# Kernel optimization log

Measured on AMD Instinct MI355X. Metric: run time of the kernel, lower is better.

## Reference

```python
import jax, jax.numpy as jnp
import numpy as np

B, C, HK, WK = 1, 128, 32, 32
S = 4                       # upsample factor hq/hk = dilation
HQ, WQ = HK * S, WK * S
NH = 4                      # heads
HD = C // NH                # head dim
KH = KW = 7                 # odd(max(3, round(2*0.1*32)))
DH = DW = S
EPS = float(jnp.finfo(jnp.float32).eps)  # torch RMSNorm default eps for fp32


def natten_indices(L, K, D):
    """NATTEN clamped-window key indices per query position. Returns [L, K] int array."""
    NS = K // 2
    i = np.arange(L)
    if D <= 1:
        start = np.maximum(i - NS, 0) + (i + NS >= L) * (L - i - NS - 1)
    else:
        ni = i - NS * D
        imodd = i % D
        a = (L // D) * D
        b = L - a
        far = np.where(imodd < b, L - b + imodd - 2 * NS * D, a + imodd - K * D)
        start = np.where(ni < 0, imodd, np.where(i + NS * D >= L, far, ni))
    return jnp.asarray(start[:, None] + np.arange(K)[None, :] * D)


def setup_inputs() -> dict:
    key = jax.random.key(0)
    ks = jax.random.split(key, 8)
    sc = 1.0 / np.sqrt(C)
    return {
        "q": jax.random.normal(ks[0], (B, C, HQ, WQ), jnp.float32),
        "k": jax.random.normal(ks[1], (B, C, HK, WK), jnp.float32),
        "v": jax.random.normal(ks[2], (B, C, HK, WK), jnp.float32),
        "conv_w": jax.random.normal(ks[3], (C, C, 3, 3), jnp.float32) * (sc / 3.0),
        "normq_w": 1.0 + 0.02 * jax.random.normal(ks[4], (C,), jnp.float32),
        "normk_w": 1.0 + 0.02 * jax.random.normal(ks[5], (C,), jnp.float32),
        "qproj_w": jax.random.normal(ks[6], (C, C), jnp.float32) * sc,
        "qproj_b": jnp.zeros((C,), jnp.float32),
        "kproj_w": jax.random.normal(ks[7], (C, C), jnp.float32) * sc,
        "kproj_b": jnp.zeros((C,), jnp.float32),
    }


def _rmsnorm(x, w):  # x: [B,C,H,W]; RMS over channel dim
    ms = jnp.mean(x * x, axis=1, keepdims=True)
    return x * jax.lax.rsqrt(ms + EPS) * w[None, :, None, None]


def reference(q, k, v, conv_w, normq_w, normk_w, qproj_w, qproj_b, kproj_w, kproj_b):
    # 3x3 conv on q (no bias, padding=1)
    q = jax.lax.conv_general_dilated(q, conv_w, (1, 1), "SAME",
                                     dimension_numbers=("NCHW", "OIHW", "NCHW"))
    q = _rmsnorm(q, normq_w)
    k = _rmsnorm(k, normk_w)
    # 1x1 projections (Conv2d k=1 with bias)
    q = jnp.einsum("oc,bchw->bohw", qproj_w, q) + qproj_b[None, :, None, None]
    k = jnp.einsum("oc,bchw->bohw", kproj_w, k) + kproj_b[None, :, None, None]
    # nearest-exact upsample of k, v to (HQ, WQ); integer factor -> exact pixel repeat
    k = jnp.repeat(jnp.repeat(k, S, axis=2), S, axis=3)
    v = jnp.repeat(jnp.repeat(v, S, axis=2), S, axis=3)
    # NATTEN layout [B, H, W, heads, hd]
    qn = q.reshape(B, NH, HD, HQ, WQ).transpose(0, 3, 4, 1, 2)
    kn = k.reshape(B, NH, HD, HQ, WQ).transpose(0, 3, 4, 1, 2)
    vh = v.transpose(0, 2, 3, 1)  # [B,HQ,WQ,C]; V is shared (expanded) across heads.
    # channel-pad-to-8 in the original is a no-op here since C % 8 == 0.
    ih = natten_indices(HQ, KH, DH)  # [HQ, KH]
    iw = natten_indices(WQ, KW, DW)  # [WQ, KW]
    k_nb = jnp.take(jnp.take(kn, ih, axis=1), iw, axis=3)  # [B,HQ,KH,WQ,KW,NH,HD]
    v_nb = jnp.take(jnp.take(vh, ih, axis=1), iw, axis=3)  # [B,HQ,KH,WQ,KW,C]
    scale = HD ** -0.5
    logits = jnp.einsum("bijhd,bimjnhd->bijhmn", qn, k_nb) * scale
    attn = jax.nn.softmax(logits.reshape(B, HQ, WQ, NH, KH * KW), axis=-1)
    attn = attn.reshape(B, HQ, WQ, NH, KH, KW)
    # heads share V, and the block takes mean over heads at the end; the mean
    # commutes with the (linear) V-contraction, so average attention first.
    attn_mean = attn.mean(axis=3)  # [B,HQ,WQ,KH,KW]
    out = jnp.einsum("bijmn,bimjnc->bcij", attn_mean, v_nb)  # [B,C,HQ,WQ]
    return out
```

## Files before the change

kernel.cpp:

```cpp
#include <hip/hip_runtime.h>

#define EPS_ 1.1920928955078125e-07f
#define SCALE_ 0.17677669529663687f

typedef __attribute__((ext_vector_type(8))) short s8b;
typedef __attribute__((ext_vector_type(4))) float f32x4;

static __device__ __forceinline__ unsigned short f2bf(float f) {
  unsigned int u = __float_as_uint(f);
  unsigned int r = (u + 0x7fffu + ((u >> 16) & 1u)) >> 16;
  return (unsigned short)r;
}
static __device__ __forceinline__ float b2fs(short h) {
  return __uint_as_float(((unsigned int)(unsigned short)h) << 16);
}
static __device__ __forceinline__ int S_(int c) {
  return (c < 3) ? 0 : ((c > 28) ? 25 : (c - 3));
}

__global__ __launch_bounds__(256) void prep_k(
    const float* __restrict__ q_in, const float* __restrict__ k_in,
    const float* __restrict__ v_in, const float* __restrict__ conv_w,
    const float* __restrict__ normq_w, const float* __restrict__ normk_w,
    const float* __restrict__ qproj_w, const float* __restrict__ kproj_w,
    const float* __restrict__ kbias,
    unsigned short* __restrict__ qb, unsigned short* __restrict__ vb,
    unsigned short* __restrict__ kpb, unsigned short* __restrict__ wb,
    unsigned short* __restrict__ wnq) {
  __shared__ __align__(16) char smem[53504];
  unsigned short* t_l = (unsigned short*)smem;
  unsigned short* x_l = (unsigned short*)smem;
  unsigned short* wnk_l = (unsigned short*)(smem + 17408);
  float* red_l = (float*)(smem + 52224);
  float* rs_l  = (float*)(smem + 53248);
  const int b = blockIdx.x, tid = threadIdx.x;
  const int w = tid >> 6, lane = tid & 63;
  const int lm = lane & 15, kg = lane >> 4;

  if (b < 256 || (b >= 265 && b < 281)) {
    const float* src = (b < 256) ? q_in : v_in;
    const int N = (b < 256) ? 16384 : 1024;
    const int px0 = (b < 256) ? b * 64 : (b - 265) * 64;
    for (int i = tid; i < 2048; i += 256) {
      int c = i >> 4, f = i & 15;
      float4 v = *(const float4*)&src[c * N + px0 + f * 4];
      t_l[(f * 4 + 0) * 136 + c] = f2bf(v.x);
      t_l[(f * 4 + 1) * 136 + c] = f2bf(v.y);
      t_l[(f * 4 + 2) * 136 + c] = f2bf(v.z);
      t_l[(f * 4 + 3) * 136 + c] = f2bf(v.w);
    }
    __syncthreads();
    if (b < 256) {
      for (int i = tid; i < 1024; i += 256) {
        int p = i >> 4, s = i & 15;
        int px = px0 + p;
        int opx = px + 2 * (px >> 7) + 131;
        *(s8b*)&qb[opx * 128 + s * 8] = *(const s8b*)&t_l[p * 136 + s * 8];
      }
    } else {
      for (int i = tid; i < 1024; i += 256) {
        int p = i >> 4, s = i & 15;
        *(s8b*)&vb[(px0 + p) * 128 + s * 8] = *(const s8b*)&t_l[p * 136 + s * 8];
      }
    }
  } else if (b < 265) {
    int gid = (b - 256) * 256 + tid;
    s8b z = {0, 0, 0, 0, 0, 0, 0, 0};
    for (int j = gid; j < 2080; j += 2304) {
      *(s8b*)&qb[j * 8] = z;
      *(s8b*)&qb[129 * 130 * 128 + j * 8] = z;
    }
    for (int j = gid; j < 2048; j += 2304) {
      int r = (j >> 4) + 1, s = j & 15;
      *(s8b*)&qb[(r * 130) * 128 + s * 8] = z;
      *(s8b*)&qb[(r * 130 + 129) * 128 + s * 8] = z;
    }
  } else if (b < 297) {
    const int px0 = (b - 281) * 64;
    for (int i = tid; i < 2048; i += 256) {
      int c = i >> 4, f = i & 15;
      float4 v = *(const float4*)&k_in[c * 1024 + px0 + f * 4];
      x_l[(f * 4 + 0) * 136 + c] = f2bf(v.x);
      x_l[(f * 4 + 1) * 136 + c] = f2bf(v.y);
      x_l[(f * 4 + 2) * 136 + c] = f2bf(v.z);
      x_l[(f * 4 + 3) * 136 + c] = f2bf(v.w);
    }
    for (int i = tid; i < 16384; i += 256) {
      int o = i >> 7, c = i & 127;
      wnk_l[o * 136 + c] = f2bf(kproj_w[i] * normk_w[c]);
    }
    __syncthreads();
    {
      int px = tid >> 2, t4 = tid & 3;
      float ssum = 0.f;
#pragma unroll
      for (int j = 0; j < 4; j++) {
        s8b v = *(const s8b*)&x_l[px * 136 + t4 * 32 + j * 8];
#pragma unroll
        for (int e = 0; e < 8; e++) { float f = b2fs(v[e]); ssum += f * f; }
      }
      red_l[px * 4 + t4] = ssum;
    }
    __syncthreads();
    if (tid < 64)
      rs_l[tid] = rsqrtf((red_l[4 * tid] + red_l[4 * tid + 1] + red_l[4 * tid + 2] +
                          red_l[4 * tid + 3]) * (1.f / 128.f) + EPS_);
    __syncthreads();
    f32x4 acc[2][4];
#pragma unroll
    for (int a = 0; a < 2; a++)
#pragma unroll
      for (int n = 0; n < 4; n++) acc[a][n] = (f32x4){0.f, 0.f, 0.f, 0.f};
#pragma unroll
    for (int kc = 0; kc < 4; kc++) {
      s8b a0 = *(const s8b*)&wnk_l[(2 * w * 16 + lm) * 136 + kc * 32 + kg * 8];
      s8b a1 = *(const s8b*)&wnk_l[((2 * w + 1) * 16 + lm) * 136 + kc * 32 + kg * 8];
#pragma unroll
      for (int nt = 0; nt < 4; nt++) {
        s8b bf = *(const s8b*)&x_l[(nt * 16 + lm) * 136 + kc * 32 + kg * 8];
        acc[0][nt] = __builtin_amdgcn_mfma_f32_16x16x32_bf16(a0, bf, acc[0][nt], 0, 0, 0);
        acc[1][nt] = __builtin_amdgcn_mfma_f32_16x16x32_bf16(a1, bf, acc[1][nt], 0, 0, 0);
      }
    }
    __syncthreads();
#pragma unroll
    for (int mi = 0; mi < 2; mi++)
#pragma unroll
      for (int nt = 0; nt < 4; nt++)
#pragma unroll
        for (int r = 0; r < 4; r++) {
          int px = nt * 16 + lm, c = (2 * w + mi) * 16 + kg * 4 + r;
          x_l[px * 136 + c] = f2bf(kbias[c] + rs_l[px] * acc[mi][nt][r]);
        }
    __syncthreads();
    for (int i = tid; i < 1024; i += 256) {
      int px = i >> 4, s = i & 15;
      *(s8b*)&kpb[(px0 + px) * 128 + s * 8] = *(const s8b*)&x_l[px * 136 + s * 8];
    }
  } else {
    int idx = (b - 297) * 256 + tid;
    if (idx < 147456) {
      int i32 = idx & 31, r = idx >> 5;
      int oc = r & 127, r2 = r >> 7;
      int kc = r2 & 3, t = r2 >> 2;
      wb[idx] = f2bf(conv_w[oc * 1152 + (kc * 32 + i32) * 9 + t]);
    } else {
      int j = idx - 147456;
      wnq[j] = f2bf(qproj_w[j] * normq_w[j & 127]);
    }
  }
}

__global__ __launch_bounds__(256) void fused_k(
    const unsigned short* __restrict__ qb, const unsigned short* __restrict__ wb,
    const unsigned short* __restrict__ wnq, const float* __restrict__ qbias,
    const unsigned short* __restrict__ kpb, const unsigned short* __restrict__ vb,
    float* __restrict__ out) {
  __shared__ __align__(16) char smem[54528];
  unsigned short* in_l = (unsigned short*)smem;
  unsigned short* qc_l = (unsigned short*)smem;
  unsigned short* a_l  = (unsigned short*)smem;
  float* o_l = (float*)smem;
  unsigned short* v_l = (unsigned short*)(smem + 34816);
  float* red_l = (float*)(smem + 53248);
  float* rs_l  = (float*)(smem + 54272);

  const int tid = threadIdx.x;
  const int CY = blockIdx.x >> 4, CX = blockIdx.x & 15;
  const int Y0 = CY * 8, X0 = CX * 8;
  const int w = tid >> 6, lane = tid & 63;
  const int lm = lane & 15, kg = lane >> 4;

  const int sy0 = S_(2 * CY), sy1 = S_(2 * CY + 1);
  const int sx0 = S_(2 * CX), sx1 = S_(2 * CX + 1);
  const int kyb = min(sy0, 24), kxb = min(sx0, 24);
  const int oy0 = sy0 - kyb, oy1 = sy1 - kyb;
  const int ox0 = sx0 - kxb, ox1 = sx1 - kxb;

  for (int i = tid; i < 1600; i += 256) {
    int s = i & 15, r = i >> 4;
    int ry = r / 10, rx = r - ry * 10;
    *(s8b*)&in_l[(ry * 12 + rx) * 136 + s * 8] =
        *(const s8b*)&qb[((Y0 + ry) * 130 + X0 + rx) * 128 + s * 8];
  }
  for (int i = tid; i < 1024; i += 256) {
    int j = i >> 4, s = i & 15;
    int ky = j >> 3, kx = j & 7;
    s8b v = *(const s8b*)&vb[((kyb + ky) * 32 + kxb + kx) * 128 + s * 8];
#pragma unroll
    for (int e = 0; e < 8; e++) v_l[(s * 8 + e) * 72 + j] = (unsigned short)v[e];
  }
  __syncthreads();

  f32x4 acc[2][4];
#pragma unroll
  for (int a = 0; a < 2; a++)
#pragma unroll
    for (int n = 0; n < 4; n++) acc[a][n] = (f32x4){0.f, 0.f, 0.f, 0.f};
#pragma unroll
  for (int t = 0; t < 9; t++) {
    const int dy = t / 3, dx = t - (t / 3) * 3;
#pragma unroll
    for (int kc = 0; kc < 4; kc++) {
      const unsigned short* wp = wb + (t * 4 + kc) * 4096;
      s8b a0 = *(const s8b*)&wp[(2 * w * 16 + lm) * 32 + kg * 8];
      s8b a1 = *(const s8b*)&wp[((2 * w + 1) * 16 + lm) * 32 + kg * 8];
#pragma unroll
      for (int nt = 0; nt < 4; nt++) {
        int qy = 2 * nt + (lm >> 3), qx = lm & 7;
        s8b bf = *(const s8b*)&in_l[((qy + dy) * 12 + qx + dx) * 136 + kc * 32 + kg * 8];
        acc[0][nt] = __builtin_amdgcn_mfma_f32_16x16x32_bf16(a0, bf, acc[0][nt], 0, 0, 0);
        acc[1][nt] = __builtin_amdgcn_mfma_f32_16x16x32_bf16(a1, bf, acc[1][nt], 0, 0, 0);
      }
    }
  }
  __syncthreads();
#pragma unroll
  for (int mi = 0; mi < 2; mi++)
#pragma unroll
    for (int nt = 0; nt < 4; nt++)
#pragma unroll
      for (int r = 0; r < 4; r++) {
        int px = nt * 16 + lm, c = (2 * w + mi) * 16 + kg * 4 + r;
        qc_l[px * 136 + c] = f2bf(acc[mi][nt][r]);
      }
  __syncthreads();

  {
    int px = tid >> 2, t4 = tid & 3;
    float ssum = 0.f;
#pragma unroll
    for (int j = 0; j < 4; j++) {
      s8b v = *(const s8b*)&qc_l[px * 136 + t4 * 32 + j * 8];
#pragma unroll
      for (int e = 0; e < 8; e++) { float f = b2fs(v[e]); ssum += f * f; }
    }
    red_l[px * 4 + t4] = ssum;
  }
  __syncthreads();
  if (tid < 64)
    rs_l[tid] = rsqrtf((red_l[4 * tid] + red_l[4 * tid + 1] + red_l[4 * tid + 2] +
                        red_l[4 * tid + 3]) * (1.f / 128.f) + EPS_);
  __syncthreads();

  f32x4 acc2[2][4];
#pragma unroll
  for (int a = 0; a < 2; a++)
#pragma unroll
    for (int n = 0; n < 4; n++) acc2[a][n] = (f32x4){0.f, 0.f, 0.f, 0.f};
#pragma unroll
  for (int kc = 0; kc < 4; kc++) {
    s8b a0 = *(const s8b*)&wnq[(2 * w * 16 + lm) * 128 + kc * 32 + kg * 8];
    s8b a1 = *(const s8b*)&wnq[((2 * w + 1) * 16 + lm) * 128 + kc * 32 + kg * 8];
#pragma unroll
    for (int nt = 0; nt < 4; nt++) {
      s8b bf = *(const s8b*)&qc_l[(nt * 16 + lm) * 136 + kc * 32 + kg * 8];
      acc2[0][nt] = __builtin_amdgcn_mfma_f32_16x16x32_bf16(a0, bf, acc2[0][nt], 0, 0, 0);
      acc2[1][nt] = __builtin_amdgcn_mfma_f32_16x16x32_bf16(a1, bf, acc2[1][nt], 0, 0, 0);
    }
  }
  __syncthreads();
#pragma unroll
  for (int mi = 0; mi < 2; mi++)
#pragma unroll
    for (int nt = 0; nt < 4; nt++)
#pragma unroll
      for (int r = 0; r < 4; r++) {
        int px = nt * 16 + lm, c = (2 * w + mi) * 16 + kg * 4 + r;
        qc_l[px * 136 + c] = f2bf(qbias[c] + rs_l[px] * acc2[mi][nt][r]);
      }
  __syncthreads();

  const int h = w;
  f32x4 lg[4][4];
  {
    s8b af[4], bf[4];
#pragma unroll
    for (int mt = 0; mt < 4; mt++)
      af[mt] = *(const s8b*)&qc_l[(mt * 16 + lm) * 136 + h * 32 + kg * 8];
#pragma unroll
    for (int nt = 0; nt < 4; nt++) {
      int n = nt * 16 + lm;
      int ky = n >> 3, kx = n & 7;
      bf[nt] = *(const s8b*)&kpb[((kyb + ky) * 32 + kxb + kx) * 128 + h * 32 + kg * 8];
    }
#pragma unroll
    for (int mt = 0; mt < 4; mt++)
#pragma unroll
      for (int nt = 0; nt < 4; nt++)
        lg[mt][nt] = __builtin_amdgcn_mfma_f32_16x16x32_bf16(
            af[mt], bf[nt], (f32x4){0.f, 0.f, 0.f, 0.f}, 0, 0, 0);
  }
  __syncthreads();

  const int kyA = lm >> 3, kxq = lm & 7;
  const bool kxv0 = (unsigned)(kxq - ox0) < 7u;
  const bool kxv1 = (unsigned)(kxq - ox1) < 7u;
#pragma unroll
  for (int mt = 0; mt < 4; mt++) {
#pragma unroll
    for (int r = 0; r < 4; r++) {
      int j = mt * 16 + kg * 4 + r;
      int oy = ((j >> 5) & 1) ? oy1 : oy0;
      bool kxv = ((j >> 2) & 1) ? kxv1 : kxv0;
      float l[4];
#pragma unroll
      for (int nt = 0; nt < 4; nt++) {
        int ky = 2 * nt + kyA;
        bool valid = kxv && ((unsigned)(ky - oy) < 7u);
        l[nt] = valid ? lg[mt][nt][r] * SCALE_ : -1e30f;
      }
      float mx = fmaxf(fmaxf(l[0], l[1]), fmaxf(l[2], l[3]));
#pragma unroll
      for (int off = 1; off < 16; off <<= 1) mx = fmaxf(mx, __shfl_xor(mx, off, 64));
      float e0 = __expf(l[0] - mx), e1 = __expf(l[1] - mx);
      float e2 = __expf(l[2] - mx), e3 = __expf(l[3] - mx);
      float ss = e0 + e1 + e2 + e3;
#pragma unroll
      for (int off = 1; off < 16; off <<= 1) ss += __shfl_xor(ss, off, 64);
      float inv = 1.f / ss;
      unsigned short* ap = &a_l[(h * 64 + j) * 68];
      ap[lm] = f2bf(e0 * inv);
      ap[16 + lm] = f2bf(e1 * inv);
      ap[32 + lm] = f2bf(e2 * inv);
      ap[48 + lm] = f2bf(e3 * inv);
    }
  }
  __syncthreads();

  f32x4 oacc[4][2];
#pragma unroll
  for (int a = 0; a < 4; a++)
#pragma unroll
    for (int n = 0; n < 2; n++) oacc[a][n] = (f32x4){0.f, 0.f, 0.f, 0.f};
#pragma unroll
  for (int kc = 0; kc < 2; kc++) {
    s8b bfr[2];
#pragma unroll
    for (int nt2 = 0; nt2 < 2; nt2++)
      bfr[nt2] = *(const s8b*)&v_l[(w * 32 + nt2 * 16 + lm) * 72 + kc * 32 + kg * 8];
#pragma unroll
    for (int hh = 0; hh < 4; hh++) {
#pragma unroll
      for (int mt = 0; mt < 4; mt++) {
        s8b afr = *(const s8b*)&a_l[(hh * 64 + mt * 16 + lm) * 68 + kc * 32 + kg * 8];
#pragma unroll
        for (int nt2 = 0; nt2 < 2; nt2++)
          oacc[mt][nt2] = __builtin_amdgcn_mfma_f32_16x16x32_bf16(afr, bfr[nt2], oacc[mt][nt2], 0, 0, 0);
      }
    }
  }
  __syncthreads();
#pragma unroll
  for (int mt = 0; mt < 4; mt++)
#pragma unroll
    for (int nt2 = 0; nt2 < 2; nt2++)
#pragma unroll
      for (int r = 0; r < 4; r++)
        o_l[(w * 32 + nt2 * 16 + lm) * 68 + mt * 16 + kg * 4 + r] = 0.25f * oacc[mt][nt2][r];
  __syncthreads();
  for (int i = tid; i < 2048; i += 256) {
    int c = i >> 4, rr = i & 15;
    int qy = rr >> 1, hx = rr & 1;
    float4 v = *(const float4*)&o_l[c * 68 + qy * 8 + hx * 4];
    *(float4*)&out[c * 16384 + (Y0 + qy) * 128 + X0 + hx * 4] = v;
  }
}

extern "C" void kernel_launch(void* const* d_in, const int* in_sizes, int n_in,
                              void* d_out, int out_size, void* d_ws, size_t ws_size,
                              hipStream_t stream) {
  const float* q_in    = (const float*)d_in[0];
  const float* k_in    = (const float*)d_in[1];
  const float* v_in    = (const float*)d_in[2];
  const float* conv_w  = (const float*)d_in[3];
  const float* normq_w = (const float*)d_in[4];
  const float* normk_w = (const float*)d_in[5];
  const float* qproj_w = (const float*)d_in[6];
  const float* qproj_b = (const float*)d_in[7];
  const float* kproj_w = (const float*)d_in[8];
  const float* kproj_b = (const float*)d_in[9];
  float* out = (float*)d_out;

  char* ws = (char*)d_ws;
  unsigned short* qb  = (unsigned short*)(ws);
  unsigned short* vb  = (unsigned short*)(ws + 4326400);
  unsigned short* kpb = (unsigned short*)(ws + 4588544);
  unsigned short* wb  = (unsigned short*)(ws + 4850688);
  unsigned short* wnq = (unsigned short*)(ws + 5145600);

  prep_k<<<dim3(937), 256, 0, stream>>>(q_in, k_in, v_in, conv_w, normq_w, normk_w,
                                        qproj_w, kproj_w, kproj_b,
                                        qb, vb, kpb, wb, wnq);
  fused_k<<<dim3(256), 256, 0, stream>>>(qb, wb, wnq, qproj_b, kpb, vb, out);
}
```

Measured before the change: 113.0 us.

## Fuse activation conversion and K projection into attention kernel, keep weight pack separate

Result: slower. 133.7 us (+18.4%).

```diff
diff --git a/kernel.cpp b/kernel.cpp
--- a/kernel.cpp
+++ b/kernel.cpp
@@ -18,158 +18,50 @@
   return (c < 3) ? 0 : ((c > 28) ? 25 : (c - 3));
 }
 
-__global__ __launch_bounds__(256) void prep_k(
+__global__ __launch_bounds__(256) void wpack_k(
+    const float* __restrict__ cw, const float* __restrict__ qw,
+    const float* __restrict__ nqw, const float* __restrict__ kw,
+    const float* __restrict__ nkw, unsigned short* __restrict__ wb,
+    unsigned short* __restrict__ wnq, unsigned short* __restrict__ wnk) {
+  int idx = blockIdx.x * 256 + threadIdx.x;
+  if (idx < 147456) {
+    int i32 = idx & 31, r = idx >> 5;
+    int oc = r & 127, r2 = r >> 7;
+    int kc = r2 & 3, t = r2 >> 2;
+    wb[idx] = f2bf(cw[oc * 1152 + (kc * 32 + i32) * 9 + t]);
+  } else if (idx < 163840) {
+    int j = idx - 147456;
+    wnq[j] = f2bf(qw[j] * nqw[j & 127]);
+  } else if (idx < 180224) {
+    int j = idx - 163840;
+    wnk[j] = f2bf(kw[j] * nkw[j & 127]);
+  }
+}
+
+__global__ __launch_bounds__(256) void fused_k(
     const float* __restrict__ q_in, const float* __restrict__ k_in,
-    const float* __restrict__ v_in, const float* __restrict__ conv_w,
-    const float* __restrict__ normq_w, const float* __restrict__ normk_w,
-    const float* __restrict__ qproj_w, const float* __restrict__ kproj_w,
-    const float* __restrict__ kbias,
-    unsigned short* __restrict__ qb, unsigned short* __restrict__ vb,
-    unsigned short* __restrict__ kpb, unsigned short* __restrict__ wb,
-    unsigned short* __restrict__ wnq) {
-  __shared__ __align__(16) char smem[53504];
-  unsigned short* t_l = (unsigned short*)smem;
-  unsigned short* x_l = (unsigned short*)smem;
-  unsigned short* wnk_l = (unsigned short*)(smem + 17408);
-  float* red_l = (float*)(smem + 52224);
-  float* rs_l  = (float*)(smem + 53248);
-  const int b = blockIdx.x, tid = threadIdx.x;
-  const int w = tid >> 6, lane = tid & 63;
-  const int lm = lane & 15, kg = lane >> 4;
-
-  if (b < 256 || (b >= 265 && b < 281)) {
-    const float* src = (b < 256) ? q_in : v_in;
-    const int N = (b < 256) ? 16384 : 1024;
-    const int px0 = (b < 256) ? b * 64 : (b - 265) * 64;
-    for (int i = tid; i < 2048; i += 256) {
-      int c = i >> 4, f = i & 15;
-      float4 v = *(const float4*)&src[c * N + px0 + f * 4];
-      t_l[(f * 4 + 0) * 136 + c] = f2bf(v.x);
-      t_l[(f * 4 + 1) * 136 + c] = f2bf(v.y);
-      t_l[(f * 4 + 2) * 136 + c] = f2bf(v.z);
-      t_l[(f * 4 + 3) * 136 + c] = f2bf(v.w);
-    }
-    __syncthreads();
-    if (b < 256) {
-      for (int i = tid; i < 1024; i += 256) {
-        int p = i >> 4, s = i & 15;
-        int px = px0 + p;
-        int opx = px + 2 * (px >> 7) + 131;
-        *(s8b*)&qb[opx * 128 + s * 8] = *(const s8b*)&t_l[p * 136 + s * 8];
-      }
-    } else {
-      for (int i = tid; i < 1024; i += 256) {
-        int p = i >> 4, s = i & 15;
-        *(s8b*)&vb[(px0 + p) * 128 + s * 8] = *(const s8b*)&t_l[p * 136 + s * 8];
-      }
-    }
-  } else if (b < 265) {
-    int gid = (b - 256) * 256 + tid;
-    s8b z = {0, 0, 0, 0, 0, 0, 0, 0};
-    for (int j = gid; j < 2080; j += 2304) {
-      *(s8b*)&qb[j * 8] = z;
-      *(s8b*)&qb[129 * 130 * 128 + j * 8] = z;
-    }
-    for (int j = gid; j < 2048; j += 2304) {
-      int r = (j >> 4) + 1, s = j & 15;
-      *(s8b*)&qb[(r * 130) * 128 + s * 8] = z;
-      *(s8b*)&qb[(r * 130 + 129) * 128 + s * 8] = z;
-    }
-  } else if (b < 297) {
-    const int px0 = (b - 281) * 64;
-    for (int i = tid; i < 2048; i += 256) {
-      int c = i >> 4, f = i & 15;
-      float4 v = *(const float4*)&k_in[c * 1024 + px0 + f * 4];
-      x_l[(f * 4 + 0) * 136 + c] = f2bf(v.x);
-      x_l[(f * 4 + 1) * 136 + c] = f2bf(v.y);
-      x_l[(f * 4 + 2) * 136 + c] = f2bf(v.z);
-      x_l[(f * 4 + 3) * 136 + c] = f2bf(v.w);
-    }
-    for (int i = tid; i < 16384; i += 256) {
-      int o = i >> 7, c = i & 127;
-      wnk_l[o * 136 + c] = f2bf(kproj_w[i] * normk_w[c]);
-    }
-    __syncthreads();
-    {
-      int px = tid >> 2, t4 = tid & 3;
-      float ssum = 0.f;
-#pragma unroll
-      for (int j = 0; j < 4; j++) {
-        s8b v = *(const s8b*)&x_l[px * 136 + t4 * 32 + j * 8];
-#pragma unroll
-        for (int e = 0; e < 8; e++) { float f = b2fs(v[e]); ssum += f * f; }
-      }
-      red_l[px * 4 + t4] = ssum;
-    }
-    __syncthreads();
-    if (tid < 64)
-      rs_l[tid] = rsqrtf((red_l[4 * tid] + red_l[4 * tid + 1] + red_l[4 * tid + 2] +
-                          red_l[4 * tid + 3]) * (1.f / 128.f) + EPS_);
-    __syncthreads();
-    f32x4 acc[2][4];
-#pragma unroll
-    for (int a = 0; a < 2; a++)
-#pragma unroll
-      for (int n = 0; n < 4; n++) acc[a][n] = (f32x4){0.f, 0.f, 0.f, 0.f};
-#pragma unroll
-    for (int kc = 0; kc < 4; kc++) {
-      s8b a0 = *(const s8b*)&wnk_l[(2 * w * 16 + lm) * 136 + kc * 32 + kg * 8];
-      s8b a1 = *(const s8b*)&wnk_l[((2 * w + 1) * 16 + lm) * 136 + kc * 32 + kg * 8];
-#pragma unroll
-      for (int nt = 0; nt < 4; nt++) {
-        s8b bf = *(const s8b*)&x_l[(nt * 16 + lm) * 136 + kc * 32 + kg * 8];
-        acc[0][nt] = __builtin_amdgcn_mfma_f32_16x16x32_bf16(a0, bf, acc[0][nt], 0, 0, 0);
-        acc[1][nt] = __builtin_amdgcn_mfma_f32_16x16x32_bf16(a1, bf, acc[1][nt], 0, 0, 0);
-      }
-    }
-    __syncthreads();
-#pragma unroll
-    for (int mi = 0; mi < 2; mi++)
-#pragma unroll
-      for (int nt = 0; nt < 4; nt++)
-#pragma unroll
-        for (int r = 0; r < 4; r++) {
-          int px = nt * 16 + lm, c = (2 * w + mi) * 16 + kg * 4 + r;
-          x_l[px * 136 + c] = f2bf(kbias[c] + rs_l[px] * acc[mi][nt][r]);
-        }
-    __syncthreads();
-    for (int i = tid; i < 1024; i += 256) {
-      int px = i >> 4, s = i & 15;
-      *(s8b*)&kpb[(px0 + px) * 128 + s * 8] = *(const s8b*)&x_l[px * 136 + s * 8];
-    }
-  } else {
-    int idx = (b - 297) * 256 + tid;
-    if (idx < 147456) {
-      int i32 = idx & 31, r = idx >> 5;
-      int oc = r & 127, r2 = r >> 7;
-      int kc = r2 & 3, t = r2 >> 2;
-      wb[idx] = f2bf(conv_w[oc * 1152 + (kc * 32 + i32) * 9 + t]);
-    } else {
-      int j = idx - 147456;
-      wnq[j] = f2bf(qproj_w[j] * normq_w[j & 127]);
-    }
-  }
-}
-
-__global__ __launch_bounds__(256) void fused_k(
-    const unsigned short* __restrict__ qb, const unsigned short* __restrict__ wb,
-    const unsigned short* __restrict__ wnq, const float* __restrict__ qbias,
-    const unsigned short* __restrict__ kpb, const unsigned short* __restrict__ vb,
+    const float* __restrict__ v_in, const unsigned short* __restrict__ wb,
+    const unsigned short* __restrict__ wnq, const unsigned short* __restrict__ wnk,
+    const float* __restrict__ qbias, const float* __restrict__ kbias,
     float* __restrict__ out) {
-  __shared__ __align__(16) char smem[54528];
+  __shared__ __align__(16) char smem[65344];
   unsigned short* in_l = (unsigned short*)smem;
   unsigned short* qc_l = (unsigned short*)smem;
-  unsigned short* a_l  = (unsigned short*)smem;
-  float* o_l = (float*)smem;
-  unsigned short* v_l = (unsigned short*)(smem + 34816);
-  float* red_l = (float*)(smem + 53248);
-  float* rs_l  = (float*)(smem + 54272);
+  unsigned short* a1_l = (unsigned short*)(smem + 17408);
+  unsigned short* kx_l = (unsigned short*)(smem + 27200);
+  unsigned short* v_l  = (unsigned short*)(smem + 44608);
+  float* o_l   = (float*)smem;
+  float* red_l = (float*)(smem + 63040);
+  float* rs_l  = (float*)(smem + 64064);
+  float* bq_l  = (float*)(smem + 64320);
+  float* bk_l  = (float*)(smem + 64832);
 
   const int tid = threadIdx.x;
   const int CY = blockIdx.x >> 4, CX = blockIdx.x & 15;
   const int Y0 = CY * 8, X0 = CX * 8;
   const int w = tid >> 6, lane = tid & 63;
   const int lm = lane & 15, kg = lane >> 4;
+  const int mg = w & 1, ng = w >> 1;
 
   const int sy0 = S_(2 * CY), sy1 = S_(2 * CY + 1);
   const int sx0 = S_(2 * CX), sx1 = S_(2 * CX + 1);
@@ -177,53 +69,25 @@
   const int oy0 = sy0 - kyb, oy1 = sy1 - kyb;
   const int ox0 = sx0 - kxb, ox1 = sx1 - kxb;
 
-  for (int i = tid; i < 1600; i += 256) {
-    int s = i & 15, r = i >> 4;
+  if (tid < 128) { bq_l[tid] = qbias[tid]; bk_l[tid] = kbias[tid]; }
+  for (int i = tid; i < 12800; i += 256) {
+    int c = i / 100, r = i - c * 100;
     int ry = r / 10, rx = r - ry * 10;
-    *(s8b*)&in_l[(ry * 12 + rx) * 136 + s * 8] =
-        *(const s8b*)&qb[((Y0 + ry) * 130 + X0 + rx) * 128 + s * 8];
-  }
-  for (int i = tid; i < 1024; i += 256) {
-    int j = i >> 4, s = i & 15;
+    int gy = Y0 - 1 + ry, gx = X0 - 1 + rx;
+    float v = 0.f;
+    if ((unsigned)gy < 128u && (unsigned)gx < 128u) v = q_in[c * 16384 + gy * 128 + gx];
+    in_l[r * 136 + c] = f2bf(v);
+  }
+  for (int i = tid; i < 8192; i += 256) {
+    int c = i >> 6, j = i & 63;
     int ky = j >> 3, kx = j & 7;
-    s8b v = *(const s8b*)&vb[((kyb + ky) * 32 + kxb + kx) * 128 + s * 8];
-#pragma unroll
-    for (int e = 0; e < 8; e++) v_l[(s * 8 + e) * 72 + j] = (unsigned short)v[e];
-  }
-  __syncthreads();
-
-  f32x4 acc[2][4];
-#pragma unroll
-  for (int a = 0; a < 2; a++)
-#pragma unroll
-    for (int n = 0; n < 4; n++) acc[a][n] = (f32x4){0.f, 0.f, 0.f, 0.f};
-#pragma unroll
-  for (int t = 0; t < 9; t++) {
-    const int dy = t / 3, dx = t - (t / 3) * 3;
-#pragma unroll
-    for (int kc = 0; kc < 4; kc++) {
-      const unsigned short* wp = wb + (t * 4 + kc) * 4096;
-      s8b a0 = *(const s8b*)&wp[(2 * w * 16 + lm) * 32 + kg * 8];
-      s8b a1 = *(const s8b*)&wp[((2 * w + 1) * 16 + lm) * 32 + kg * 8];
-#pragma unroll
-      for (int nt = 0; nt < 4; nt++) {
-        int qy = 2 * nt + (lm >> 3), qx = lm & 7;
-        s8b bf = *(const s8b*)&in_l[((qy + dy) * 12 + qx + dx) * 136 + kc * 32 + kg * 8];
-        acc[0][nt] = __builtin_amdgcn_mfma_f32_16x16x32_bf16(a0, bf, acc[0][nt], 0, 0, 0);
-        acc[1][nt] = __builtin_amdgcn_mfma_f32_16x16x32_bf16(a1, bf, acc[1][nt], 0, 0, 0);
-      }
-    }
-  }
-  __syncthreads();
-#pragma unroll
-  for (int mi = 0; mi < 2; mi++)
-#pragma unroll
-    for (int nt = 0; nt < 4; nt++)
-#pragma unroll
-      for (int r = 0; r < 4; r++) {
-        int px = nt * 16 + lm, c = (2 * w + mi) * 16 + kg * 4 + r;
-        qc_l[px * 136 + c] = f2bf(acc[mi][nt][r]);
-      }
+    kx_l[j * 136 + c] = f2bf(k_in[c * 1024 + (kyb + ky) * 32 + kxb + kx]);
+  }
+  for (int i = tid; i < 8192; i += 256) {
+    int c = i >> 6, j = i & 63;
+    int ky = j >> 3, kx = j & 7;
+    v_l[c * 72 + j] = f2bf(v_in[c * 1024 + (kyb + ky) * 32 + kxb + kx]);
+  }
   __syncthreads();
 
   {
@@ -231,7 +95,7 @@
     float ssum = 0.f;
 #pragma unroll
     for (int j = 0; j < 4; j++) {
-      s8b v = *(const s8b*)&qc_l[px * 136 + t4 * 32 + j * 8];
+      s8b v = *(const s8b*)&kx_l[px * 136 + t4 * 32 + j * 8];
 #pragma unroll
       for (int e = 0; e < 8; e++) { float f = b2fs(v[e]); ssum += f * f; }
     }
@@ -243,56 +107,150 @@
                         red_l[4 * tid + 3]) * (1.f / 128.f) + EPS_);
   __syncthreads();
 
-  f32x4 acc2[2][4];
-#pragma unroll
-  for (int a = 0; a < 2; a++)
-#pragma unroll
-    for (int n = 0; n < 4; n++) acc2[a][n] = (f32x4){0.f, 0.f, 0.f, 0.f};
-#pragma unroll
-  for (int kc = 0; kc < 4; kc++) {
-    s8b a0 = *(const s8b*)&wnq[(2 * w * 16 + lm) * 128 + kc * 32 + kg * 8];
-    s8b a1 = *(const s8b*)&wnq[((2 * w + 1) * 16 + lm) * 128 + kc * 32 + kg * 8];
-#pragma unroll
-    for (int nt = 0; nt < 4; nt++) {
-      s8b bf = *(const s8b*)&qc_l[(nt * 16 + lm) * 136 + kc * 32 + kg * 8];
-      acc2[0][nt] = __builtin_amdgcn_mfma_f32_16x16x32_bf16(a0, bf, acc2[0][nt], 0, 0, 0);
-      acc2[1][nt] = __builtin_amdgcn_mfma_f32_16x16x32_bf16(a1, bf, acc2[1][nt], 0, 0, 0);
-    }
-  }
-  __syncthreads();
-#pragma unroll
-  for (int mi = 0; mi < 2; mi++)
-#pragma unroll
-    for (int nt = 0; nt < 4; nt++)
+  {
+    f32x4 ka[4][2];
+#pragma unroll
+    for (int a = 0; a < 4; a++)
+#pragma unroll
+      for (int n = 0; n < 2; n++) ka[a][n] = (f32x4){0.f, 0.f, 0.f, 0.f};
+#pragma unroll
+    for (int kc = 0; kc < 4; kc++) {
+      s8b af[4], bf[2];
+#pragma unroll
+      for (int mt = 0; mt < 4; mt++)
+        af[mt] = *(const s8b*)&wnk[((mg * 4 + mt) * 16 + lm) * 128 + kc * 32 + kg * 8];
+#pragma unroll
+      for (int nt = 0; nt < 2; nt++)
+        bf[nt] = *(const s8b*)&kx_l[((ng * 2 + nt) * 16 + lm) * 136 + kc * 32 + kg * 8];
+#pragma unroll
+      for (int mt = 0; mt < 4; mt++)
+#pragma unroll
+        for (int nt = 0; nt < 2; nt++)
+          ka[mt][nt] = __builtin_amdgcn_mfma_f32_16x16x32_bf16(af[mt], bf[nt], ka[mt][nt], 0, 0, 0);
+    }
+    __syncthreads();
+#pragma unroll
+    for (int mt = 0; mt < 4; mt++)
+#pragma unroll
+      for (int nt = 0; nt < 2; nt++)
+#pragma unroll
+        for (int r = 0; r < 4; r++) {
+          int px = (ng * 2 + nt) * 16 + lm, c = (mg * 4 + mt) * 16 + kg * 4 + r;
+          kx_l[px * 136 + c] = f2bf(bk_l[c] + rs_l[px] * ka[mt][nt][r]);
+        }
+  }
+  __syncthreads();
+
+  f32x4 acc[4][2];
+#pragma unroll
+  for (int a = 0; a < 4; a++)
+#pragma unroll
+    for (int n = 0; n < 2; n++) acc[a][n] = (f32x4){0.f, 0.f, 0.f, 0.f};
+#pragma unroll
+  for (int t = 0; t < 9; t++) {
+    const int dy = t / 3, dx = t - (t / 3) * 3;
+#pragma unroll
+    for (int kc = 0; kc < 4; kc++) {
+      const unsigned short* wp = wb + (t * 4 + kc) * 4096;
+      s8b af[4], bf[2];
+#pragma unroll
+      for (int mt = 0; mt < 4; mt++)
+        af[mt] = *(const s8b*)&wp[((mg * 4 + mt) * 16 + lm) * 32 + kg * 8];
+#pragma unroll
+      for (int nt = 0; nt < 2; nt++) {
+        int px = (ng * 2 + nt) * 16 + lm;
+        int qy = px >> 3, qx = px & 7;
+        bf[nt] = *(const s8b*)&in_l[((qy + dy) * 10 + qx + dx) * 136 + kc * 32 + kg * 8];
+      }
+#pragma unroll
+      for (int mt = 0; mt < 4; mt++)
+#pragma unroll
+        for (int nt = 0; nt < 2; nt++)
+          acc[mt][nt] = __builtin_amdgcn_mfma_f32_16x16x32_bf16(af[mt], bf[nt], acc[mt][nt], 0, 0, 0);
+    }
+  }
+  __syncthreads();
+#pragma unroll
+  for (int mt = 0; mt < 4; mt++)
+#pragma unroll
+    for (int nt = 0; nt < 2; nt++)
 #pragma unroll
       for (int r = 0; r < 4; r++) {
-        int px = nt * 16 + lm, c = (2 * w + mi) * 16 + kg * 4 + r;
-        qc_l[px * 136 + c] = f2bf(qbias[c] + rs_l[px] * acc2[mi][nt][r]);
+        int px = (ng * 2 + nt) * 16 + lm, c = (mg * 4 + mt) * 16 + kg * 4 + r;
+        qc_l[px * 136 + c] = f2bf(acc[mt][nt][r]);
       }
+  __syncthreads();
+
+  {
+    int px = tid >> 2, t4 = tid & 3;
+    float ssum = 0.f;
+#pragma unroll
+    for (int j = 0; j < 4; j++) {
+      s8b v = *(const s8b*)&qc_l[px * 136 + t4 * 32 + j * 8];
+#pragma unroll
+      for (int e = 0; e < 8; e++) { float f = b2fs(v[e]); ssum += f * f; }
+    }
+    red_l[px * 4 + t4] = ssum;
+  }
+  __syncthreads();
+  if (tid < 64)
+    rs_l[tid] = rsqrtf((red_l[4 * tid] + red_l[4 * tid + 1] + red_l[4 * tid + 2] +
+                        red_l[4 * tid + 3]) * (1.f / 128.f) + EPS_);
+  __syncthreads();
+
+  {
+    f32x4 qa[4][2];
+#pragma unroll
+    for (int a = 0; a < 4; a++)
+#pragma unroll
+      for (int n = 0; n < 2; n++) qa[a][n] = (f32x4){0.f, 0.f, 0.f, 0.f};
+#pragma unroll
+    for (int kc = 0; kc < 4; kc++) {
+      s8b af[4], bf[2];
+#pragma unroll
+      for (int mt = 0; mt < 4; mt++)
+        af[mt] = *(const s8b*)&wnq[((mg * 4 + mt) * 16 + lm) * 128 + kc * 32 + kg * 8];
+#pragma unroll
+      for (int nt = 0; nt < 2; nt++)
+        bf[nt] = *(const s8b*)&qc_l[((ng * 2 + nt) * 16 + lm) * 136 + kc * 32 + kg * 8];
+#pragma unroll
+      for (int mt = 0; mt < 4; mt++)
+#pragma unroll
+        for (int nt = 0; nt < 2; nt++)
+          qa[mt][nt] = __builtin_amdgcn_mfma_f32_16x16x32_bf16(af[mt], bf[nt], qa[mt][nt], 0, 0, 0);
+    }
+    __syncthreads();
+#pragma unroll
+    for (int mt = 0; mt < 4; mt++)
+#pragma unroll
+      for (int nt = 0; nt < 2; nt++)
+#pragma unroll
+        for (int r = 0; r < 4; r++) {
+          int px = (ng * 2 + nt) * 16 + lm, c = (mg * 4 + mt) * 16 + kg * 4 + r;
+          qc_l[px * 136 + c] = f2bf(bq_l[c] + rs_l[px] * qa[mt][nt][r]);
+        }
+  }
   __syncthreads();
 
   const int h = w;
   f32x4 lg[4][4];
   {
-    s8b af[4], bf[4];
+    s8b qa[4], kb[4];
 #pragma unroll
     for (int mt = 0; mt < 4; mt++)
-      af[mt] = *(const s8b*)&qc_l[(mt * 16 + lm) * 136 + h * 32 + kg * 8];
-#pragma unroll
-    for (int nt = 0; nt < 4; nt++) {
-      int n = nt * 16 + lm;
-      int ky = n >> 3, kx = n & 7;
-      bf[nt] = *(const s8b*)&kpb[((kyb + ky) * 32 + kxb + kx) * 128 + h * 32 + kg * 8];
-    }
+      qa[mt] = *(const s8b*)&qc_l[(mt * 16 + lm) * 136 + h * 32 + kg * 8];
+#pragma unroll
+    for (int nt = 0; nt < 4; nt++)
+      kb[nt] = *(const s8b*)&kx_l[(nt * 16 + lm) * 136 + h * 32 + kg * 8];
 #pragma unroll
     for (int mt = 0; mt < 4; mt++)
 #pragma unroll
       for (int nt = 0; nt < 4; nt++)
         lg[mt][nt] = __builtin_amdgcn_mfma_f32_16x16x32_bf16(
-            af[mt], bf[nt], (f32x4){0.f, 0.f, 0.f, 0.f}, 0, 0, 0);
-  }
-  __syncthreads();
-
+            qa[mt], kb[nt], (f32x4){0.f, 0.f, 0.f, 0.f}, 0, 0, 0);
+  }
+
+  unsigned int pk[4][4][2];
   const int kyA = lm >> 3, kxq = lm & 7;
   const bool kxv0 = (unsigned)(kxq - ox0) < 7u;
   const bool kxv1 = (unsigned)(kxq - ox1) < 7u;
@@ -319,14 +277,10 @@
 #pragma unroll
       for (int off = 1; off < 16; off <<= 1) ss += __shfl_xor(ss, off, 64);
       float inv = 1.f / ss;
-      unsigned short* ap = &a_l[(h * 64 + j) * 68];
-      ap[lm] = f2bf(e0 * inv);
-      ap[16 + lm] = f2bf(e1 * inv);
-      ap[32 + lm] = f2bf(e2 * inv);
-      ap[48 + lm] = f2bf(e3 * inv);
-    }
-  }
-  __syncthreads();
+      pk[mt][r][0] = (unsigned)f2bf(e0 * inv) | ((unsigned)f2bf(e1 * inv) << 16);
+      pk[mt][r][1] = (unsigned)f2bf(e2 * inv) | ((unsigned)f2bf(e3 * inv) << 16);
+    }
+  }
 
   f32x4 oacc[4][2];
 #pragma unroll
@@ -334,23 +288,39 @@
 #pragma unroll
     for (int n = 0; n < 2; n++) oacc[a][n] = (f32x4){0.f, 0.f, 0.f, 0.f};
 #pragma unroll
-  for (int kc = 0; kc < 2; kc++) {
-    s8b bfr[2];
-#pragma unroll
-    for (int nt2 = 0; nt2 < 2; nt2++)
-      bfr[nt2] = *(const s8b*)&v_l[(w * 32 + nt2 * 16 + lm) * 72 + kc * 32 + kg * 8];
-#pragma unroll
-    for (int hh = 0; hh < 4; hh++) {
-#pragma unroll
-      for (int mt = 0; mt < 4; mt++) {
-        s8b afr = *(const s8b*)&a_l[(hh * 64 + mt * 16 + lm) * 68 + kc * 32 + kg * 8];
+  for (int hh = 0; hh < 4; hh++) {
+    __syncthreads();
+    if (w == hh) {
+#pragma unroll
+      for (int mt = 0; mt < 4; mt++)
+#pragma unroll
+        for (int r = 0; r < 4; r++) {
+          int j = mt * 16 + kg * 4 + r;
+          a1_l[j * 72 + lm]      = (unsigned short)(pk[mt][r][0] & 0xffffu);
+          a1_l[j * 72 + 16 + lm] = (unsigned short)(pk[mt][r][0] >> 16);
+          a1_l[j * 72 + 32 + lm] = (unsigned short)(pk[mt][r][1] & 0xffffu);
+          a1_l[j * 72 + 48 + lm] = (unsigned short)(pk[mt][r][1] >> 16);
+        }
+    }
+    __syncthreads();
+#pragma unroll
+    for (int kc = 0; kc < 2; kc++) {
+      s8b pa[4], vb2[2];
+#pragma unroll
+      for (int mt = 0; mt < 4; mt++)
+        pa[mt] = *(const s8b*)&a1_l[(mt * 16 + lm) * 72 + kc * 32 + kg * 8];
+#pragma unroll
+      for (int nt2 = 0; nt2 < 2; nt2++)
+        vb2[nt2] = *(const s8b*)&v_l[(w * 32 + nt2 * 16 + lm) * 72 + kc * 32 + kg * 8];
+#pragma unroll
+      for (int mt = 0; mt < 4; mt++)
 #pragma unroll
         for (int nt2 = 0; nt2 < 2; nt2++)
-          oacc[mt][nt2] = __builtin_amdgcn_mfma_f32_16x16x32_bf16(afr, bfr[nt2], oacc[mt][nt2], 0, 0, 0);
-      }
-    }
-  }
-  __syncthreads();
+          oacc[mt][nt2] = __builtin_amdgcn_mfma_f32_16x16x32_bf16(pa[mt], vb2[nt2], oacc[mt][nt2], 0, 0, 0);
+    }
+  }
+  __syncthreads();
+
 #pragma unroll
   for (int mt = 0; mt < 4; mt++)
 #pragma unroll
@@ -383,14 +353,12 @@
   float* out = (float*)d_out;
 
   char* ws = (char*)d_ws;
-  unsigned short* qb  = (unsigned short*)(ws);
-  unsigned short* vb  = (unsigned short*)(ws + 4326400);
-  unsigned short* kpb = (unsigned short*)(ws + 4588544);
-  unsigned short* wb  = (unsigned short*)(ws + 4850688);
-  unsigned short* wnq = (unsigned short*)(ws + 5145600);
-
-  prep_k<<<dim3(937), 256, 0, stream>>>(q_in, k_in, v_in, conv_w, normq_w, normk_w,
-                                        qproj_w, kproj_w, kproj_b,
-                                        qb, vb, kpb, wb, wnq);
-  fused_k<<<dim3(256), 256, 0, stream>>>(qb, wb, wnq, qproj_b, kpb, vb, out);
-}
+  unsigned short* wb  = (unsigned short*)(ws);
+  unsigned short* wnq = (unsigned short*)(ws + 294912);
+  unsigned short* wnk = (unsigned short*)(ws + 327680);
+
+  wpack_k<<<dim3(704), 256, 0, stream>>>(conv_w, qproj_w, normq_w, kproj_w, normk_w,
+                                         wb, wnq, wnk);
+  fused_k<<<dim3(256), 256, 0, stream>>>(q_in, k_in, v_in, wb, wnq, wnk,
+                                         qproj_b, kproj_b, out);
+}
```
